# Optimization experiments

Hardware: AMD Instinct MI355X
Metric: run time of the kernel (lower is better)

The kernel has to match this reference:

```python
import jax, jax.numpy as jnp
import numpy as np

GAMMA1, GAMMA2, GAMMA3 = 4.0, 5.0, 10.0
BSIZE = 5
EPS = 1e-10


def _l2norm(x, axis):
    # torch F.normalize: x / max(||x||2, 1e-12)
    n = jnp.sqrt(jnp.sum(x * x, axis=axis, keepdims=True))
    return x / jnp.maximum(n, 1e-12)


def _block_score(v, e, M, HW):
    """calculate_matching_score for one block with uniform segment length.
    v: [B, R, D] flattened image regions (R = M*HW); e: [B, L, D] per-sample texts.
    Segments of the concatenated text are the B chunks of length L (lenAry cumulative).
    """
    B, R, D = v.shape
    L = e.shape[1]
    Tb = B * L
    ef = e.reshape(Tb, D)
    vf = v.reshape(B * R, D)
    s = vf @ ef.T                                        # [B*R, Tb]
    # per-text-segment softmax over text dim, then scale by gamma1
    s_nt = GAMMA1 * jax.nn.softmax(s.reshape(B * R, B, L), axis=-1)
    # attention over image regions
    alpha = jax.nn.softmax(s_nt.reshape(B, R, Tb), axis=1)
    v_tidal = jnp.einsum('brt,brd->btd', alpha, v)       # [B, Tb, D]
    logit = jnp.sum(_l2norm(v_tidal, 2) * _l2norm(ef, 1)[None], axis=2)  # [B, Tb]
    score1 = jnp.sum(jnp.exp(logit).reshape(B, B, L), axis=2)            # [B, B]
    lsm1 = jnp.log(score1 ** (1.0 / GAMMA2) + EPS)
    # beta path: softmax over all regions, exp, reduce over spatial cells
    s_nt2 = jax.nn.softmax(s.reshape(B, R, Tb), axis=1).reshape(B, M, HW, Tb)
    s_exp = jnp.exp(s_nt2)
    sd = jnp.sum(s_exp, axis=2)                          # [B, M, Tb]
    sd4 = sd.reshape(B, M, B, L)
    sd_seg = jnp.sum(sd4, axis=3, keepdims=True)         # per-segment denominators
    beta = sd4 / sd_seg                                  # [B, M, B, L] (= sum_hw s_exp / sd_rep)
    em = jnp.einsum('bmsl,sld->bmsd', beta, e)           # [B, M, B, D] (em_prime)
    # em is constant over the HW repeat axis, so the mean of dot products collapses:
    v_norm_sum = jnp.sum(_l2norm(v.reshape(B, M, HW, D), 3), axis=2)     # [B, M, D]
    logit2 = jnp.einsum('bmsd,bmd->bms', _l2norm(em, 3), v_norm_sum) / HW  # [B, M, B]
    score2 = jnp.sum(jnp.exp(logit2), axis=1) ** (1.0 / GAMMA2)          # [B, B]
    lsm2 = jnp.log(score2 + EPS)
    # beta decorrelation regularizer
    beta_f = beta.reshape(B, M, Tb)
    tmp = jnp.einsum('bmt,bnt->bmn', beta_f, beta_f)     # [B, M, M]
    off = tmp * (1.0 - jnp.eye(M, dtype=tmp.dtype))
    loss_reg = jnp.mean(jnp.sqrt(jnp.sum(off * off, axis=(1, 2))))
    lsm = GAMMA3 * (lsm1 + lsm2)
    d = jnp.diagonal(lsm)
    pdq = -jnp.sum(jnp.log(d / jnp.sum(lsm, axis=1) + EPS))
    pqd = -jnp.sum(jnp.log(d / jnp.sum(lsm, axis=0) + EPS))
    return (pdq + pqd) / B + loss_reg


def setup_inputs() -> dict:
    key = jax.random.key(0)
    k1, k2 = jax.random.split(key)
    B, M, D, H_r, H_w, L = 40, 8, 256, 16, 16, 15
    image = jax.random.normal(k1, (B, M, D, H_r, H_w), dtype=jnp.float32)
    text = jax.random.normal(k2, (B, L, D), dtype=jnp.float32)
    length_info = jnp.full((B,), L, dtype=jnp.int32)  # uniform lengths (max = 15)
    return {'image': image, 'text': text, 'length_info': length_info}


def reference(image, text, length_info):
    B, M, D, H_r, H_w = image.shape
    HW = H_r * H_w
    R = M * HW
    # (shuffle omitted for determinism; identity permutation)
    img = jnp.transpose(image, (0, 1, 3, 4, 2)).reshape(B, R, D)
    nblk = B // BSIZE
    v_blocks = img.reshape(nblk, BSIZE, R, D)
    e_blocks = text.reshape(nblk, BSIZE, text.shape[1], D)
    scores = jax.vmap(lambda v, e: _block_score(v, e, M, HW))(v_blocks, e_blocks)
    numBlcks = B // BSIZE + 1  # faithful to int(B/bsize)+1 in the source
    return jnp.sum(scores) / numBlcks
```

## Files before the change

### kernel.cpp

```cpp
#include <hip/hip_runtime.h>
#include <hip/hip_bf16.h>
#include <math.h>

#define NG 8
#define NB5 5
#define NM 8
#define NHW 256
#define NR 2048
#define ND 256
#define NL 15
#define NT 75
#define NGB 40

#define OFF_S    0
#define SZ_S     (NGB*NT*NR)
#define OFF_W    (OFF_S + SZ_S)
#define OFF_RMAX (OFF_W + SZ_S)
#define SZ_RST   (NGB*5*NR)
#define OFF_RSUM (OFF_RMAX + SZ_RST)
#define OFF_SD   (OFF_RSUM + SZ_RST)
#define SZ_SD    (NGB*NM*NT)
#define OFF_VNS  (OFF_SD + SZ_SD)
#define SZ_VNS   (NGB*NM*ND)
#define OFF_LG   (OFF_VNS + SZ_VNS)
#define SZ_LG    (NGB*NT)
#define OFF_LG2  (OFF_LG + SZ_LG)
#define SZ_LG2   (NGB*NM*5)
#define OFF_BETA (OFF_LG2 + SZ_LG2)
#define SZ_BETA  (NGB*NM*NT)
#define OFF_BLK  (OFF_BETA + SZ_BETA)

#define SHFL_TAIL_ADD(V)                                                       \
    V += __shfl_down(V, 32); V += __shfl_down(V, 16); V += __shfl_down(V, 8);  \
    V += __shfl_down(V, 4);  V += __shfl_down(V, 2);  V += __shfl_down(V, 1);
#define SHFL_TAIL_MAX(V)                                                       \
    V = fmaxf(V, __shfl_down(V, 32)); V = fmaxf(V, __shfl_down(V, 16));        \
    V = fmaxf(V, __shfl_down(V, 8));  V = fmaxf(V, __shfl_down(V, 4));         \
    V = fmaxf(V, __shfl_down(V, 2));  V = fmaxf(V, __shfl_down(V, 1));

__global__ __launch_bounds__(256, 2) void k1_gemm_s(const float* __restrict__ image,
                                                    const float* __restrict__ text,
                                                    float* __restrict__ ws) {
    __shared__ __align__(16) float A[32][260];
    __shared__ __align__(16) float Et[32][52];
    float* Sg = ws + OFF_S;
    int blk = blockIdx.x;
    int th = blk >= 320 ? 1 : 0;
    int rest = blk - th * 320;
    int m = rest & 7, gb = rest >> 3;
    int g = gb / 5;
    int tb = th * 40;
    const float* cell = image + (size_t)(gb * 8 + m) * ND * NHW;
    int tid = threadIdx.x;
    int lane = tid & 63;
    int w = __builtin_amdgcn_readfirstlane(tid >> 6);
    int hw4 = lane * 4;
    int arow = tid >> 6;
    int acol = (tid & 63) * 4;
    int edd  = tid & 31;
    int etc0 = tid >> 5;
    float4 acc[10];
#pragma unroll
    for (int j = 0; j < 10; ++j) acc[j] = make_float4(0.f, 0.f, 0.f, 0.f);
    float4 p0, p1, p2, p3, p4, p5, p6, p7;
    float e0, e1, e2, e3, e4;
    const float* tbase = text + (size_t)g * 75 * 256;
#define K1_T(I) ((tb + etc0 + 8 * (I)) > 74 ? 74 : (tb + etc0 + 8 * (I)))
#define K1_LOAD(D0)                                                              \
    p0 = *(const float4*)&cell[(size_t)((D0) + arow +  0) * 256 + acol];         \
    p1 = *(const float4*)&cell[(size_t)((D0) + arow +  4) * 256 + acol];         \
    p2 = *(const float4*)&cell[(size_t)((D0) + arow +  8) * 256 + acol];         \
    p3 = *(const float4*)&cell[(size_t)((D0) + arow + 12) * 256 + acol];         \
    p4 = *(const float4*)&cell[(size_t)((D0) + arow + 16) * 256 + acol];         \
    p5 = *(const float4*)&cell[(size_t)((D0) + arow + 20) * 256 + acol];         \
    p6 = *(const float4*)&cell[(size_t)((D0) + arow + 24) * 256 + acol];         \
    p7 = *(const float4*)&cell[(size_t)((D0) + arow + 28) * 256 + acol];         \
    e0 = tbase[(size_t)K1_T(0) * 256 + (D0) + edd];                              \
    e1 = tbase[(size_t)K1_T(1) * 256 + (D0) + edd];                              \
    e2 = tbase[(size_t)K1_T(2) * 256 + (D0) + edd];                              \
    e3 = tbase[(size_t)K1_T(3) * 256 + (D0) + edd];                              \
    e4 = tbase[(size_t)K1_T(4) * 256 + (D0) + edd];
#define K1_ECOL(I) (((etc0 + 8 * (I)) / 10) * 12 + ((etc0 + 8 * (I)) % 10))
    K1_LOAD(0)
    for (int c = 0; c < 8; ++c) {
        __syncthreads();
        *(float4*)&A[arow +  0][acol] = p0;
        *(float4*)&A[arow +  4][acol] = p1;
        *(float4*)&A[arow +  8][acol] = p2;
        *(float4*)&A[arow + 12][acol] = p3;
        *(float4*)&A[arow + 16][acol] = p4;
        *(float4*)&A[arow + 20][acol] = p5;
        *(float4*)&A[arow + 24][acol] = p6;
        *(float4*)&A[arow + 28][acol] = p7;
        Et[edd][K1_ECOL(0)] = e0;
        Et[edd][K1_ECOL(1)] = e1;
        Et[edd][K1_ECOL(2)] = e2;
        Et[edd][K1_ECOL(3)] = e3;
        Et[edd][K1_ECOL(4)] = e4;
        __syncthreads();
        if (c < 7) { K1_LOAD((c + 1) * 32) }
        for (int dd = 0; dd < 32; ++dd) {
            float4 av = *(const float4*)&A[dd][hw4];
            float4 q0 = *(const float4*)&Et[dd][w * 12];
            float4 q1 = *(const float4*)&Et[dd][w * 12 + 4];
            float2 q2 = *(const float2*)&Et[dd][w * 12 + 8];
            float ev[10] = {q0.x, q0.y, q0.z, q0.w, q1.x, q1.y, q1.z, q1.w, q2.x, q2.y};
#pragma unroll
            for (int j = 0; j < 10; ++j) {
                acc[j].x += av.x * ev[j]; acc[j].y += av.y * ev[j];
                acc[j].z += av.z * ev[j]; acc[j].w += av.w * ev[j];
            }
        }
    }
#undef K1_LOAD
#undef K1_T
#undef K1_ECOL
#pragma unroll
    for (int j = 0; j < 10; ++j) {
        int t = tb + w * 10 + j;
        if (t < 75)
            *(float4*)&Sg[((size_t)gb * 75 + t) * 2048 + m * 256 + hw4] = acc[j];
    }
}

__global__ __launch_bounds__(256) void k2_rowstats(float* __restrict__ ws) {
    const float* Sg = ws + OFF_S;
    float* RMAX = ws + OFF_RMAX;
    float* RSUM = ws + OFF_RSUM;
    int blk = blockIdx.x;
    int m = blk & 7, gb = blk >> 3;
    int r = m * 256 + threadIdx.x;
    const float* base = Sg + (size_t)gb * 75 * 2048 + r;
    for (int seg = 0; seg < 5; ++seg) {
        float v[15]; float mx = -1e30f;
#pragma unroll
        for (int l = 0; l < 15; ++l) {
            v[l] = base[(size_t)(seg * 15 + l) * 2048];
            mx = fmaxf(mx, v[l]);
        }
        float sm = 0.f;
#pragma unroll
        for (int l = 0; l < 15; ++l) sm += __expf(v[l] - mx);
        RMAX[((size_t)gb * 5 + seg) * 2048 + r] = mx;
        RSUM[((size_t)gb * 5 + seg) * 2048 + r] = sm;
    }
}

__global__ __launch_bounds__(256) void k3_colstats(float* __restrict__ ws) {
    __shared__ float redA[256];
    __shared__ float redB[256];
    __shared__ float red8[8][256];
    __shared__ float bc[2];
    const float* Sg = ws + OFF_S;
    const float* RMAX = ws + OFF_RMAX;
    const float* RSUM = ws + OFF_RSUM;
    float* W = ws + OFF_W;
    float* SD = ws + OFF_SD;
    int blk = blockIdx.x;
    int t = blk % 75, gb = blk / 75;
    int seg = t / 15;
    int tid = threadIdx.x;
    const float* col = Sg + ((size_t)gb * 75 + t) * 2048;
    const float* rmx = RMAX + ((size_t)gb * 5 + seg) * 2048;
    const float* rsm = RSUM + ((size_t)gb * 5 + seg) * 2048;
    float sv[8], ent[8];
    float lmax = -1e30f, lsnt = 0.f;
#pragma unroll
    for (int k = 0; k < 8; ++k) {
        int r = tid + 256 * k;
        float s = col[r];
        sv[k] = s;
        float snt = 4.f * __expf(s - rmx[r]) / rsm[r];
        float e = __expf(snt);
        ent[k] = e;
        lsnt += e;
        lmax = fmaxf(lmax, s);
    }
    redA[tid] = lmax; __syncthreads();
    if (tid < 128) redA[tid] = fmaxf(redA[tid], redA[tid + 128]);
    __syncthreads();
    if (tid < 64) {
        float v = fmaxf(redA[tid], redA[tid + 64]);
        SHFL_TAIL_MAX(v)
        if (tid == 0) bc[0] = v;
    }
    __syncthreads();
    float cmax = bc[0];
    float pe[8]; float lse = 0.f;
#pragma unroll
    for (int k = 0; k < 8; ++k) { pe[k] = __expf(sv[k] - cmax); lse += pe[k]; }
    redA[tid] = lse; redB[tid] = lsnt; __syncthreads();
    if (tid < 128) { redA[tid] += redA[tid + 128]; redB[tid] += redB[tid + 128]; }
    __syncthreads();
    if (tid < 64) {
        float a = redA[tid] + redA[tid + 64];
        float b = redB[tid] + redB[tid + 64];
        SHFL_TAIL_ADD(a)
        SHFL_TAIL_ADD(b)
        if (tid == 0) { bc[0] = 1.f / b; bc[1] = 1.f / a; }
    }
    __syncthreads();
    float inv = bc[0], icsum = bc[1];
#pragma unroll
    for (int k = 0; k < 8; ++k)
        W[((size_t)gb * 75 + t) * 2048 + tid + 256 * k] = ent[k] * inv;
#pragma unroll
    for (int k = 0; k < 8; ++k) red8[k][tid] = __expf(pe[k] * icsum);
    __syncthreads();
    if (tid < 128) {
#pragma unroll
        for (int k = 0; k < 8; ++k) red8[k][tid] += red8[k][tid + 128];
    }
    __syncthreads();
    if (tid < 64) {
        float v[8];
#pragma unroll
        for (int k = 0; k < 8; ++k) v[k] = red8[k][tid] + red8[k][tid + 64];
#pragma unroll
        for (int k = 0; k < 8; ++k) { SHFL_TAIL_ADD(v[k]) }
        if (tid == 0) {
#pragma unroll
            for (int k = 0; k < 8; ++k)
                SD[((size_t)gb * 8 + k) * 75 + t] = v[k];
        }
    }
}

__global__ __launch_bounds__(256, 2) void k4_vtidal(const float* __restrict__ image,
                                                    float* __restrict__ ws) {
    __shared__ __align__(16) float V[32][260];
    __shared__ __align__(16) float WtT[32][52];
    const float* W = ws + OFF_W;
    float* VTP = ws + OFF_S;
    int blk = blockIdx.x;
    int th = blk >= 320 ? 1 : 0;
    int rest = blk - th * 320;
    int m = rest & 7, gb = rest >> 3;
    int tb = th * 40;
    const float* cell = image + (size_t)(gb * 8 + m) * ND * NHW;
    int tid = threadIdx.x;
    int lane = tid & 63;
    int w = __builtin_amdgcn_readfirstlane(tid >> 6);
    int d4 = lane * 4;
    int rr4  = (tid & 7) * 4;
    int drow = tid >> 3;
    int wrr  = tid & 31;
    int wtc0 = tid >> 5;
    float4 acc[10];
#pragma unroll
    for (int j = 0; j < 10; ++j) acc[j] = make_float4(0.f, 0.f, 0.f, 0.f);
    const float* wb = W + (size_t)gb * 75 * 2048 + m * 256;
    float4 p0, p1, p2, p3, p4, p5, p6, p7;
    float w0, w1, w2, w3, w4;
#define K4_T(I) ((tb + wtc0 + 8 * (I)) > 74 ? 74 : (tb + wtc0 + 8 * (I)))
#define K4_LOAD(RC)                                                               \
    p0 = *(const float4*)&cell[(size_t)(drow +   0) * 256 + (RC) * 32 + rr4];     \
    p1 = *(const float4*)&cell[(size_t)(drow +  32) * 256 + (RC) * 32 + rr4];     \
    p2 = *(const float4*)&cell[(size_t)(drow +  64) * 256 + (RC) * 32 + rr4];     \
    p3 = *(const float4*)&cell[(size_t)(drow +  96) * 256 + (RC) * 32 + rr4];     \
    p4 = *(const float4*)&cell[(size_t)(drow + 128) * 256 + (RC) * 32 + rr4];     \
    p5 = *(const float4*)&cell[(size_t)(drow + 160) * 256 + (RC) * 32 + rr4];     \
    p6 = *(const float4*)&cell[(size_t)(drow + 192) * 256 + (RC) * 32 + rr4];     \
    p7 = *(const float4*)&cell[(size_t)(drow + 224) * 256 + (RC) * 32 + rr4];     \
    w0 = wb[(size_t)K4_T(0) * 2048 + (RC) * 32 + wrr];                            \
    w1 = wb[(size_t)K4_T(1) * 2048 + (RC) * 32 + wrr];                            \
    w2 = wb[(size_t)K4_T(2) * 2048 + (RC) * 32 + wrr];                            \
    w3 = wb[(size_t)K4_T(3) * 2048 + (RC) * 32 + wrr];                            \
    w4 = wb[(size_t)K4_T(4) * 2048 + (RC) * 32 + wrr];
#define K4_WCOL(I) (((wtc0 + 8 * (I)) / 10) * 12 + ((wtc0 + 8 * (I)) % 10))
#define K4_VST(P, DOFF)                                                           \
    V[rr4 + 0][drow + (DOFF)] = (P).x;                                            \
    V[rr4 + 1][drow + (DOFF)] = (P).y;                                            \
    V[rr4 + 2][drow + (DOFF)] = (P).z;                                            \
    V[rr4 + 3][drow + (DOFF)] = (P).w;
    K4_LOAD(0)
    for (int rc = 0; rc < 8; ++rc) {
        __syncthreads();
        K4_VST(p0,   0) K4_VST(p1,  32) K4_VST(p2,  64) K4_VST(p3,  96)
        K4_VST(p4, 128) K4_VST(p5, 160) K4_VST(p6, 192) K4_VST(p7, 224)
        WtT[wrr][K4_WCOL(0)] = w0;
        WtT[wrr][K4_WCOL(1)] = w1;
        WtT[wrr][K4_WCOL(2)] = w2;
        WtT[wrr][K4_WCOL(3)] = w3;
        WtT[wrr][K4_WCOL(4)] = w4;
        __syncthreads();
        if (rc < 7) { K4_LOAD(rc + 1) }
        for (int rr = 0; rr < 32; ++rr) {
            float4 vv = *(const float4*)&V[rr][d4];
            float4 q0 = *(const float4*)&WtT[rr][w * 12];
            float4 q1 = *(const float4*)&WtT[rr][w * 12 + 4];
            float2 q2 = *(const float2*)&WtT[rr][w * 12 + 8];
            float wv[10] = {q0.x, q0.y, q0.z, q0.w, q1.x, q1.y, q1.z, q1.w, q2.x, q2.y};
#pragma unroll
            for (int j = 0; j < 10; ++j) {
                acc[j].x += vv.x * wv[j]; acc[j].y += vv.y * wv[j];
                acc[j].z += vv.z * wv[j]; acc[j].w += vv.w * wv[j];
            }
        }
    }
#undef K4_LOAD
#undef K4_T
#undef K4_WCOL
#undef K4_VST
#pragma unroll
    for (int j = 0; j < 10; ++j) {
        int t = tb + w * 10 + j;
        if (t < 75)
            *(float4*)&VTP[((size_t)(gb * 8 + m) * 75 + t) * 256 + d4] = acc[j];
    }
}

__global__ __launch_bounds__(256) void k5_logit(const float* __restrict__ text,
                                                float* __restrict__ ws) {
    __shared__ float rA[256], rB[256], rC[256];
    const float* VTP = ws + OFF_S;
    float* LG = ws + OFF_LG;
    int blk = blockIdx.x;
    int t = blk % 75, gb = blk / 75, g = gb / 5;
    int tid = threadIdx.x;
    float vt = 0.f;
#pragma unroll
    for (int m = 0; m < 8; ++m)
        vt += VTP[((size_t)(gb * 8 + m) * 75 + t) * 256 + tid];
    int seg = t / 15, l = t % 15;
    float ev = text[((size_t)(g * 5 + seg) * 15 + l) * 256 + tid];
    rA[tid] = vt * vt; rB[tid] = ev * ev; rC[tid] = vt * ev;
    __syncthreads();
    if (tid < 128) {
        rA[tid] += rA[tid + 128];
        rB[tid] += rB[tid + 128];
        rC[tid] += rC[tid + 128];
    }
    __syncthreads();
    if (tid < 64) {
        float a = rA[tid] + rA[tid + 64];
        float b = rB[tid] + rB[tid + 64];
        float c = rC[tid] + rC[tid + 64];
        SHFL_TAIL_ADD(a)
        SHFL_TAIL_ADD(b)
        SHFL_TAIL_ADD(c)
        if (tid == 0)
            LG[gb * 75 + t] = c / (fmaxf(sqrtf(a), 1e-12f) * fmaxf(sqrtf(b), 1e-12f));
    }
}

__global__ __launch_bounds__(256) void k6_vns(const float* __restrict__ image,
                                              float* __restrict__ ws) {
    __shared__ float A[32][257];
    __shared__ float rn[256];
    __shared__ float ps[256];
    float* VNS = ws + OFF_VNS;
    int blk = blockIdx.x;
    int m = blk & 7, gb = blk >> 3;
    const float* cell = image + (size_t)(gb * 8 + m) * ND * NHW;
    int tid = threadIdx.x;
    float nsq = 0.f;
    for (int d = 0; d < 256; ++d) {
        float v = cell[d * 256 + tid];
        nsq += v * v;
    }
    rn[tid] = 1.f / fmaxf(sqrtf(nsq), 1e-12f);
    int d_loc = tid & 31, sub = tid >> 5;
    for (int d0 = 0; d0 < 256; d0 += 32) {
        __syncthreads();
#pragma unroll
        for (int i = 0; i < 32; ++i) A[i][tid] = cell[(d0 + i) * 256 + tid];
        __syncthreads();
        float partial = 0.f;
#pragma unroll
        for (int k = 0; k < 32; ++k) {
            int hw = sub + 8 * k;
            partial += A[d_loc][hw] * rn[hw];
        }
        ps[tid] = partial; __syncthreads();
        if (tid < 128) ps[tid] += ps[tid + 128];
        __syncthreads();
        if (tid < 64) ps[tid] += ps[tid + 64];
        __syncthreads();
        if (tid < 32)
            VNS[((size_t)gb * 8 + m) * 256 + d0 + tid] = ps[tid] + ps[tid + 32];
    }
}

__global__ __launch_bounds__(256) void k7_em(const float* __restrict__ text,
                                             float* __restrict__ ws) {
    __shared__ float rA[256], rB[256];
    __shared__ float sdv[75];
    __shared__ float segs[5];
    __shared__ float betas[5][15];
    const float* SD = ws + OFF_SD;
    const float* VNS = ws + OFF_VNS;
    float* BETA = ws + OFF_BETA;
    float* LG2 = ws + OFF_LG2;
    int blk = blockIdx.x;
    int m = blk & 7, gb = blk >> 3, g = gb / 5;
    int tid = threadIdx.x;
    if (tid < 75) sdv[tid] = SD[((size_t)gb * 8 + m) * 75 + tid];
    __syncthreads();
    if (tid < 5) {
        float s = 0.f;
        for (int l = 0; l < 15; ++l) s += sdv[tid * 15 + l];
        segs[tid] = s;
    }
    __syncthreads();
    if (tid < 75) {
        float b = sdv[tid] / segs[tid / 15];
        betas[tid / 15][tid % 15] = b;
        BETA[((size_t)gb * 8 + m) * 75 + tid] = b;
    }
    __syncthreads();
    float vns = VNS[((size_t)gb * 8 + m) * 256 + tid];
    for (int s = 0; s < 5; ++s) {
        float em = 0.f;
#pragma unroll
        for (int l = 0; l < 15; ++l)
            em += betas[s][l] * text[((size_t)(g * 5 + s) * 15 + l) * 256 + tid];
        rA[tid] = em * em; rB[tid] = em * vns;
        __syncthreads();
        if (tid < 128) { rA[tid] += rA[tid + 128]; rB[tid] += rB[tid + 128]; }
        __syncthreads();
        if (tid < 64) {
            float a = rA[tid] + rA[tid + 64];
            float b = rB[tid] + rB[tid + 64];
            SHFL_TAIL_ADD(a)
            SHFL_TAIL_ADD(b)
            if (tid == 0)
                LG2[((size_t)gb * 8 + m) * 5 + s] =
                    b / fmaxf(sqrtf(a), 1e-12f) * (1.f / 256.f);
        }
        __syncthreads();
    }
}

__global__ __launch_bounds__(256) void k8_final(float* __restrict__ ws) {
    __shared__ float lsm[5][5];
    __shared__ float offsq[5][64];
    __shared__ float regs[5];
    const float* LG = ws + OFF_LG;
    const float* LG2 = ws + OFF_LG2;
    const float* BETA = ws + OFF_BETA;
    float* BLK = ws + OFF_BLK;
    int g = blockIdx.x;
    int tid = threadIdx.x;
    if (tid < 25) {
        int b = tid / 5, s = tid % 5;
        int gb = g * 5 + b;
        float s1 = 0.f;
        for (int l = 0; l < 15; ++l) s1 += expf(LG[gb * 75 + s * 15 + l]);
        float s2 = 0.f;
        for (int mm = 0; mm < 8; ++mm) s2 += expf(LG2[((size_t)gb * 8 + mm) * 5 + s]);
        float l1 = logf(powf(s1, 0.2f) + 1e-10f);
        float l2 = logf(powf(s2, 0.2f) + 1e-10f);
        lsm[b][s] = 10.f * (l1 + l2);
    }
    for (int p = tid; p < 320; p += 256) {
        int b = p >> 6, mn = p & 63, mm = mn >> 3, nn = mn & 7;
        int gb = g * 5 + b;
        const float* bm = BETA + ((size_t)gb * 8 + mm) * 75;
        const float* bn = BETA + ((size_t)gb * 8 + nn) * 75;
        float acc = 0.f;
        for (int t2 = 0; t2 < 75; ++t2) acc += bm[t2] * bn[t2];
        offsq[b][mn] = (mm == nn) ? 0.f : acc * acc;
    }
    __syncthreads();
    if (tid < 5) {
        float s = 0.f;
        for (int i = 0; i < 64; ++i) s += offsq[tid][i];
        regs[tid] = sqrtf(s);
    }
    __syncthreads();
    if (tid == 0) {
        float loss_reg = 0.f;
        for (int b = 0; b < 5; ++b) loss_reg += regs[b];
        loss_reg *= 0.2f;
        float pdq = 0.f, pqd = 0.f;
        for (int i = 0; i < 5; ++i) {
            float rsum = 0.f, csum = 0.f;
            for (int j = 0; j < 5; ++j) { rsum += lsm[i][j]; csum += lsm[j][i]; }
            float di = lsm[i][i];
            pdq += -logf(di / rsum + 1e-10f);
            pqd += -logf(di / csum + 1e-10f);
        }
        BLK[g] = (pdq + pqd) * 0.2f + loss_reg;
    }
}

__global__ void k9_out(const float* __restrict__ ws, float* __restrict__ out) {
    if (threadIdx.x == 0) {
        float s = 0.f;
        for (int g2 = 0; g2 < 8; ++g2) s += ws[OFF_BLK + g2];
        out[0] = s / 9.f;
    }
}

extern "C" void kernel_launch(void* const* d_in, const int* in_sizes, int n_in,
                              void* d_out, int out_size, void* d_ws, size_t ws_size,
                              hipStream_t stream) {
    const float* image = (const float*)d_in[0];
    const float* text  = (const float*)d_in[1];
    float* ws = (float*)d_ws;
    float* out = (float*)d_out;
    hipLaunchKernelGGL(k1_gemm_s,   dim3(640),  dim3(256), 0, stream, image, text, ws);
    hipLaunchKernelGGL(k2_rowstats, dim3(320),  dim3(256), 0, stream, ws);
    hipLaunchKernelGGL(k3_colstats, dim3(3000), dim3(256), 0, stream, ws);
    hipLaunchKernelGGL(k4_vtidal,   dim3(640),  dim3(256), 0, stream, image, ws);
    hipLaunchKernelGGL(k5_logit,    dim3(3000), dim3(256), 0, stream, text, ws);
    hipLaunchKernelGGL(k6_vns,      dim3(320),  dim3(256), 0, stream, image, ws);
    hipLaunchKernelGGL(k7_em,       dim3(320),  dim3(256), 0, stream, text, ws);
    hipLaunchKernelGGL(k8_final,    dim3(8),    dim3(256), 0, stream, ws);
    hipLaunchKernelGGL(k9_out,      dim3(1),    dim3(64),  0, stream, ws, out);
}
```

Baseline: 286.4 us.

## Fuse region norms into GEMM, split rowstats per segment, swizzle vtidal LDS

Three changes. First, the first GEMM kernel now accumulates each region's squared norm from the tile it already holds in shared memory and writes it to the VNS slot. The norm kernel then reads that value instead of re-streaming the whole image column. Second, the row-statistics kernel gives each segment its own block, launching five times more blocks to raise parallelism. Third, the vtidal shared-memory tile drops its padding for an XOR swizzle to avoid bank conflicts. The risk is that the norm kernel now depends on the VNS buffer written by the first kernel; it reads the squared norm before overwriting that buffer later, which appears consistent.

```diff
diff --git a/kernel.cpp b/kernel.cpp
--- a/kernel.cpp
+++ b/kernel.cpp
@@ -62,6 +62,7 @@
     float4 acc[10];
 #pragma unroll
     for (int j = 0; j < 10; ++j) acc[j] = make_float4(0.f, 0.f, 0.f, 0.f);
+    float4 nsqa = make_float4(0.f, 0.f, 0.f, 0.f);
     float4 p0, p1, p2, p3, p4, p5, p6, p7;
     float e0, e1, e2, e3, e4;
     const float* tbase = text + (size_t)g * 75 * 256;
@@ -101,6 +102,8 @@
         if (c < 7) { K1_LOAD((c + 1) * 32) }
         for (int dd = 0; dd < 32; ++dd) {
             float4 av = *(const float4*)&A[dd][hw4];
+            nsqa.x += av.x * av.x; nsqa.y += av.y * av.y;
+            nsqa.z += av.z * av.z; nsqa.w += av.w * av.w;
             float4 q0 = *(const float4*)&Et[dd][w * 12];
             float4 q1 = *(const float4*)&Et[dd][w * 12 + 4];
             float2 q2 = *(const float2*)&Et[dd][w * 12 + 8];
@@ -121,6 +124,8 @@
         if (t < 75)
             *(float4*)&Sg[((size_t)gb * 75 + t) * 2048 + m * 256 + hw4] = acc[j];
     }
+    if (th == 0 && w == 0)
+        *(float4*)&ws[OFF_VNS + (size_t)(gb * 8 + m) * 256 + hw4] = nsqa;
 }
 
 __global__ __launch_bounds__(256) void k2_rowstats(float* __restrict__ ws) {
@@ -128,22 +133,22 @@
     float* RMAX = ws + OFF_RMAX;
     float* RSUM = ws + OFF_RSUM;
     int blk = blockIdx.x;
-    int m = blk & 7, gb = blk >> 3;
-    int r = m * 256 + threadIdx.x;
+    int chunk = blk & 7;
+    int rest = blk >> 3;
+    int seg = rest % 5, gb = rest / 5;
+    int r = chunk * 256 + threadIdx.x;
     const float* base = Sg + (size_t)gb * 75 * 2048 + r;
-    for (int seg = 0; seg < 5; ++seg) {
-        float v[15]; float mx = -1e30f;
-#pragma unroll
-        for (int l = 0; l < 15; ++l) {
-            v[l] = base[(size_t)(seg * 15 + l) * 2048];
-            mx = fmaxf(mx, v[l]);
-        }
-        float sm = 0.f;
-#pragma unroll
-        for (int l = 0; l < 15; ++l) sm += __expf(v[l] - mx);
-        RMAX[((size_t)gb * 5 + seg) * 2048 + r] = mx;
-        RSUM[((size_t)gb * 5 + seg) * 2048 + r] = sm;
-    }
+    float v[15]; float mx = -1e30f;
+#pragma unroll
+    for (int l = 0; l < 15; ++l) {
+        v[l] = base[(size_t)(seg * 15 + l) * 2048];
+        mx = fmaxf(mx, v[l]);
+    }
+    float sm = 0.f;
+#pragma unroll
+    for (int l = 0; l < 15; ++l) sm += __expf(v[l] - mx);
+    RMAX[((size_t)gb * 5 + seg) * 2048 + r] = mx;
+    RSUM[((size_t)gb * 5 + seg) * 2048 + r] = sm;
 }
 
 __global__ __launch_bounds__(256) void k3_colstats(float* __restrict__ ws) {
@@ -228,7 +233,7 @@
 
 __global__ __launch_bounds__(256, 2) void k4_vtidal(const float* __restrict__ image,
                                                     float* __restrict__ ws) {
-    __shared__ __align__(16) float V[32][260];
+    __shared__ __align__(16) float V[32 * 256];
     __shared__ __align__(16) float WtT[32][52];
     const float* W = ws + OFF_W;
     float* VTP = ws + OFF_S;
@@ -268,11 +273,12 @@
     w3 = wb[(size_t)K4_T(3) * 2048 + (RC) * 32 + wrr];                            \
     w4 = wb[(size_t)K4_T(4) * 2048 + (RC) * 32 + wrr];
 #define K4_WCOL(I) (((wtc0 + 8 * (I)) / 10) * 12 + ((wtc0 + 8 * (I)) % 10))
+#define K4_VADDR(RR, D) (((RR) << 8) + ((((D) >> 2) ^ (((RR) >> 2) & 7)) << 2) + ((D) & 3))
 #define K4_VST(P, DOFF)                                                           \
-    V[rr4 + 0][drow + (DOFF)] = (P).x;                                            \
-    V[rr4 + 1][drow + (DOFF)] = (P).y;                                            \
-    V[rr4 + 2][drow + (DOFF)] = (P).z;                                            \
-    V[rr4 + 3][drow + (DOFF)] = (P).w;
+    V[K4_VADDR(rr4 + 0, drow + (DOFF))] = (P).x;                                  \
+    V[K4_VADDR(rr4 + 1, drow + (DOFF))] = (P).y;                                  \
+    V[K4_VADDR(rr4 + 2, drow + (DOFF))] = (P).z;                                  \
+    V[K4_VADDR(rr4 + 3, drow + (DOFF))] = (P).w;
     K4_LOAD(0)
     for (int rc = 0; rc < 8; ++rc) {
         __syncthreads();
@@ -286,7 +292,8 @@
         __syncthreads();
         if (rc < 7) { K4_LOAD(rc + 1) }
         for (int rr = 0; rr < 32; ++rr) {
-            float4 vv = *(const float4*)&V[rr][d4];
+            int sr = (rr >> 2) & 7;
+            float4 vv = *(const float4*)&V[(rr << 8) + ((lane ^ sr) << 2)];
             float4 q0 = *(const float4*)&WtT[rr][w * 12];
             float4 q1 = *(const float4*)&WtT[rr][w * 12 + 4];
             float2 q2 = *(const float2*)&WtT[rr][w * 12 + 8];
@@ -301,6 +308,7 @@
 #undef K4_LOAD
 #undef K4_T
 #undef K4_WCOL
+#undef K4_VADDR
 #undef K4_VST
 #pragma unroll
     for (int j = 0; j < 10; ++j) {
@@ -354,11 +362,7 @@
     int m = blk & 7, gb = blk >> 3;
     const float* cell = image + (size_t)(gb * 8 + m) * ND * NHW;
     int tid = threadIdx.x;
-    float nsq = 0.f;
-    for (int d = 0; d < 256; ++d) {
-        float v = cell[d * 256 + tid];
-        nsq += v * v;
-    }
+    float nsq = VNS[((size_t)gb * 8 + m) * 256 + tid];
     rn[tid] = 1.f / fmaxf(sqrtf(nsq), 1e-12f);
     int d_loc = tid & 31, sub = tid >> 5;
     for (int d0 = 0; d0 < 256; d0 += 32) {
@@ -501,7 +505,7 @@
     float* ws = (float*)d_ws;
     float* out = (float*)d_out;
     hipLaunchKernelGGL(k1_gemm_s,   dim3(640),  dim3(256), 0, stream, image, text, ws);
-    hipLaunchKernelGGL(k2_rowstats, dim3(320),  dim3(256), 0, stream, ws);
+    hipLaunchKernelGGL(k2_rowstats, dim3(1600), dim3(256), 0, stream, ws);
     hipLaunchKernelGGL(k3_colstats, dim3(3000), dim3(256), 0, stream, ws);
     hipLaunchKernelGGL(k4_vtidal,   dim3(640),  dim3(256), 0, stream, image, ws);
     hipLaunchKernelGGL(k5_logit,    dim3(3000), dim3(256), 0, stream, text, ws);
```

After: 272.5 us. 4.9% less time.
